# Performance work log

Hardware: AMD Instinct MI355X
Metric: run time of the kernel (lower is better)

## Reference

```python
import jax, jax.numpy as jnp
import numpy as np

B, N, K, C_IN, C_OUT = 8, 24576, 16, 64, 64
BN_EPS = 1e-5


def setup_inputs() -> dict:
    key = jax.random.key(0)
    k1, k2, k3, k4, k5 = jax.random.split(key, 5)
    x = jax.random.normal(k1, (B, N, C_IN), dtype=jnp.float32)
    W = jax.random.normal(k2, (C_OUT, C_IN), dtype=jnp.float32) * 0.05  # Linear weight (no bias)
    # BN affine params; module inits gamma to `init` (0.0) but that zeroes the output,
    # so we use a perturbed gamma for a meaningful correctness baseline.
    gamma = 1.0 + 0.1 * jax.random.normal(k3, (C_OUT,), dtype=jnp.float32)
    beta = 0.1 * jax.random.normal(k4, (C_OUT,), dtype=jnp.float32)
    knn = jax.random.randint(k5, (B, N, K), 0, N, dtype=jnp.int32)
    return {"x": x, "W": W, "gamma": gamma, "beta": beta, "knn": knn}


def _vector_feature(h, knn):
    # h: [B, N, C], knn: [B, N, K] -> max over neighbors of (h_j - h_i): [B, N, C]
    b, n, k = knn.shape
    nbr = jnp.take_along_axis(h, knn.reshape(b, n * k, 1), axis=1).reshape(b, n, k, -1)
    return jnp.max(nbr - h[:, :, None, :], axis=2)


def reference(x, W, gamma, beta, knn):
    h = jnp.einsum('bnc,oc->bno', x, W)            # linear, no bias
    v = _vector_feature(h, knn)                    # knn edge max-pool
    # BatchNorm1d in training mode: batch stats over B*N rows, per channel
    mean = jnp.mean(v, axis=(0, 1))
    var = jnp.mean(jnp.square(v - mean), axis=(0, 1))  # biased variance
    out = (v - mean) * jax.lax.rsqrt(var + BN_EPS) * gamma + beta
    return out
```

## Files before the change

### kernel.cpp

```cpp
#include <hip/hip_runtime.h>
#include <hip/hip_bf16.h>

static constexpr int Bc   = 8;
static constexpr int Nn   = 24576;
static constexpr int Kk   = 16;
static constexpr int Cc   = 64;
static constexpr int Rr   = Bc * Nn;
static constexpr float EPS = 1e-5f;

__global__ __launch_bounds__(256) void linear_kernel(
    const float* __restrict__ x, const float* __restrict__ W,
    __hip_bfloat16* __restrict__ h)
{
    __shared__ float xs[16][64];
    const int tid  = threadIdx.x;
    const int lane = tid & 63;
    const int wave = tid >> 6;

    float w[64];
#pragma unroll
    for (int c4 = 0; c4 < 16; ++c4) {
        float4 t = *reinterpret_cast<const float4*>(&W[lane * 64 + c4 * 4]);
        w[c4 * 4 + 0] = t.x; w[c4 * 4 + 1] = t.y;
        w[c4 * 4 + 2] = t.z; w[c4 * 4 + 3] = t.w;
    }

    const int ntiles = Rr / 16;
    for (int tile = blockIdx.x; tile < ntiles; tile += gridDim.x) {
        const int row0 = tile * 16;
        reinterpret_cast<float4*>(&xs[0][0])[tid] =
            reinterpret_cast<const float4*>(&x[row0 * 64])[tid];
        __syncthreads();
#pragma unroll
        for (int rr = 0; rr < 4; ++rr) {
            const int r = wave * 4 + rr;
            float acc = 0.f;
#pragma unroll
            for (int c4 = 0; c4 < 16; ++c4) {
                float4 t = *reinterpret_cast<const float4*>(&xs[r][c4 * 4]);
                acc = fmaf(t.x, w[c4 * 4 + 0], acc);
                acc = fmaf(t.y, w[c4 * 4 + 1], acc);
                acc = fmaf(t.z, w[c4 * 4 + 2], acc);
                acc = fmaf(t.w, w[c4 * 4 + 3], acc);
            }
            h[(row0 + r) * 64 + lane] = __float2bfloat16(acc);
        }
        __syncthreads();
    }
}

__global__ __launch_bounds__(256) void gather_bn_kernel(
    const __hip_bfloat16* __restrict__ h, const int* __restrict__ knn,
    float* __restrict__ v, float* __restrict__ stats)
{
    const int tid   = threadIdx.x;
    const int lane  = tid & 63;
    const int wave  = tid >> 6;
    const int gwave = blockIdx.x * 4 + wave;
    const int nwav  = gridDim.x * 4;

    float lsum = 0.f, lsq = 0.f;

    for (int row = gwave; row < Rr; row += nwav) {
        const int b     = row / Nn;
        const int bbase = b * Nn;
        const int idx   = knn[row * Kk + (lane & 15)];
        const float hown = __bfloat162float(h[row * 64 + lane]);
        float m = -1e30f;
#pragma unroll
        for (int k = 0; k < Kk; ++k) {
            const int j = __shfl(idx, k);
            m = fmaxf(m, __bfloat162float(h[(bbase + j) * 64 + lane]));
        }
        const float val = m - hown;
        v[row * 64 + lane] = val;
        lsum += val;
        lsq  += val * val;
    }

    __shared__ float s_sum[4][64];
    __shared__ float s_sq[4][64];
    s_sum[wave][lane] = lsum;
    s_sq[wave][lane]  = lsq;
    __syncthreads();
    if (wave == 0) {
        const float a = s_sum[0][lane] + s_sum[1][lane] + s_sum[2][lane] + s_sum[3][lane];
        const float q = s_sq[0][lane]  + s_sq[1][lane]  + s_sq[2][lane]  + s_sq[3][lane];
        atomicAdd(&stats[lane], a);
        atomicAdd(&stats[64 + lane], q);
    }
}

__global__ __launch_bounds__(64) void finalize_stats_kernel(
    const float* __restrict__ stats, const float* __restrict__ gamma,
    const float* __restrict__ beta, float* __restrict__ ss)
{
    const int o = threadIdx.x;
    const float inv_count = 1.0f / (float)Rr;
    const float mean = stats[o] * inv_count;
    const float var  = stats[64 + o] * inv_count - mean * mean;
    const float sc   = gamma[o] * rsqrtf(var + EPS);
    ss[o]      = sc;
    ss[64 + o] = beta[o] - mean * sc;
}

__global__ __launch_bounds__(256) void norm_kernel(
    float* __restrict__ v, const float* __restrict__ ss)
{
    __shared__ float sc[64], sh[64];
    if (threadIdx.x < 64) {
        sc[threadIdx.x] = ss[threadIdx.x];
        sh[threadIdx.x] = ss[64 + threadIdx.x];
    }
    __syncthreads();

    const int total4 = Rr * 64 / 4;
    for (int i = blockIdx.x * blockDim.x + threadIdx.x; i < total4;
         i += gridDim.x * blockDim.x) {
        float4 t = reinterpret_cast<float4*>(v)[i];
        const int c = (i * 4) & 63;
        t.x = t.x * sc[c + 0] + sh[c + 0];
        t.y = t.y * sc[c + 1] + sh[c + 1];
        t.z = t.z * sc[c + 2] + sh[c + 2];
        t.w = t.w * sc[c + 3] + sh[c + 3];
        reinterpret_cast<float4*>(v)[i] = t;
    }
}

extern "C" void kernel_launch(void* const* d_in, const int* in_sizes, int n_in,
                              void* d_out, int out_size, void* d_ws, size_t ws_size,
                              hipStream_t stream)
{
    const float* x     = (const float*)d_in[0];
    const float* W     = (const float*)d_in[1];
    const float* gamma = (const float*)d_in[2];
    const float* beta  = (const float*)d_in[3];
    const int*   knn   = (const int*)d_in[4];
    float*       out   = (float*)d_out;

    __hip_bfloat16* h = (__hip_bfloat16*)d_ws;
    float* stats = (float*)((char*)d_ws + (size_t)Rr * 64 * sizeof(__hip_bfloat16));
    float* ss    = stats + 128;

    hipMemsetAsync(stats, 0, 128 * sizeof(float), stream);

    linear_kernel<<<1024, 256, 0, stream>>>(x, W, h);
    gather_bn_kernel<<<2048, 256, 0, stream>>>(h, knn, out, stats);
    finalize_stats_kernel<<<1, 64, 0, stream>>>(stats, gamma, beta, ss);
    norm_kernel<<<2048, 256, 0, stream>>>(out, ss);
}
```

Before: 237.8 us.

## Use bf16 MFMA for linear, bf16 intermediate v, two-row gather, nontemporal IO

The linear layer is replaced by a per-wave bf16 MFMA 16x16x32 kernel that takes its A fragments straight from global memory, removing the shared-memory staging and scalar FMA loop. The gather kernel now handles two rows per wave iteration to expose more memory-level parallelism and writes v as bf16 into the workspace instead of fp32. The norm kernel reads the bf16 v and writes fp32 output with nontemporal stores. This cuts intermediate traffic, at the cost of extra bf16 rounding on x, W and v, which lowers accuracy.

```diff
diff --git a/kernel.cpp b/kernel.cpp
--- a/kernel.cpp
+++ b/kernel.cpp
@@ -1,5 +1,9 @@
 #include <hip/hip_runtime.h>
 #include <hip/hip_bf16.h>
+
+typedef short s16x8 __attribute__((ext_vector_type(8)));
+typedef float f32x4 __attribute__((ext_vector_type(4)));
+typedef unsigned short u16x8 __attribute__((ext_vector_type(8)));
 
 static constexpr int Bc   = 8;
 static constexpr int Nn   = 24576;
@@ -8,50 +12,83 @@
 static constexpr int Rr   = Bc * Nn;
 static constexpr float EPS = 1e-5f;
 
-__global__ __launch_bounds__(256) void linear_kernel(
+__device__ __forceinline__ unsigned short f2bf(float f) {
+    union { float f; unsigned int u; } c; c.f = f;
+    unsigned int r = c.u + 0x7FFFu + ((c.u >> 16) & 1u);
+    return (unsigned short)(r >> 16);
+}
+__device__ __forceinline__ float bf2f(unsigned short u) {
+    union { unsigned int u; float f; } c; c.u = ((unsigned int)u) << 16; return c.f;
+}
+
+__global__ __launch_bounds__(256) void linear_mfma_kernel(
     const float* __restrict__ x, const float* __restrict__ W,
     __hip_bfloat16* __restrict__ h)
 {
-    __shared__ float xs[16][64];
     const int tid  = threadIdx.x;
-    const int lane = tid & 63;
+    const int l    = tid & 63;
     const int wave = tid >> 6;
-
-    float w[64];
-#pragma unroll
-    for (int c4 = 0; c4 < 16; ++c4) {
-        float4 t = *reinterpret_cast<const float4*>(&W[lane * 64 + c4 * 4]);
-        w[c4 * 4 + 0] = t.x; w[c4 * 4 + 1] = t.y;
-        w[c4 * 4 + 2] = t.z; w[c4 * 4 + 3] = t.w;
-    }
-
+    const int gwave = blockIdx.x * 4 + wave;
+    const int nwav  = gridDim.x * 4;
+
+    const int lr = l & 15;
+    const int kg = (l >> 4) * 8;
+    const int dr = (l >> 4) * 4;
+
+    s16x8 bfrag[4][2];
+#pragma unroll
+    for (int ct = 0; ct < 4; ++ct)
+#pragma unroll
+        for (int kc = 0; kc < 2; ++kc) {
+            const float* bp = W + (ct * 16 + lr) * 64 + kc * 32 + kg;
+            f32x4 b0 = *reinterpret_cast<const f32x4*>(bp);
+            f32x4 b1 = *reinterpret_cast<const f32x4*>(bp + 4);
+            s16x8 f;
+            f[0] = (short)f2bf(b0[0]); f[1] = (short)f2bf(b0[1]);
+            f[2] = (short)f2bf(b0[2]); f[3] = (short)f2bf(b0[3]);
+            f[4] = (short)f2bf(b1[0]); f[5] = (short)f2bf(b1[1]);
+            f[6] = (short)f2bf(b1[2]); f[7] = (short)f2bf(b1[3]);
+            bfrag[ct][kc] = f;
+        }
+
+    unsigned short* hu = (unsigned short*)h;
     const int ntiles = Rr / 16;
-    for (int tile = blockIdx.x; tile < ntiles; tile += gridDim.x) {
-        const int row0 = tile * 16;
-        reinterpret_cast<float4*>(&xs[0][0])[tid] =
-            reinterpret_cast<const float4*>(&x[row0 * 64])[tid];
-        __syncthreads();
-#pragma unroll
-        for (int rr = 0; rr < 4; ++rr) {
-            const int r = wave * 4 + rr;
-            float acc = 0.f;
-#pragma unroll
-            for (int c4 = 0; c4 < 16; ++c4) {
-                float4 t = *reinterpret_cast<const float4*>(&xs[r][c4 * 4]);
-                acc = fmaf(t.x, w[c4 * 4 + 0], acc);
-                acc = fmaf(t.y, w[c4 * 4 + 1], acc);
-                acc = fmaf(t.z, w[c4 * 4 + 2], acc);
-                acc = fmaf(t.w, w[c4 * 4 + 3], acc);
-            }
-            h[(row0 + r) * 64 + lane] = __float2bfloat16(acc);
+    for (int t = gwave; t < ntiles; t += nwav) {
+        const int row0 = t * 16;
+        const float* ap = x + (row0 + lr) * 64 + kg;
+        f32x4 a0 = *reinterpret_cast<const f32x4*>(ap);
+        f32x4 a1 = *reinterpret_cast<const f32x4*>(ap + 4);
+        f32x4 a2 = *reinterpret_cast<const f32x4*>(ap + 32);
+        f32x4 a3 = *reinterpret_cast<const f32x4*>(ap + 36);
+        s16x8 fa0, fa1;
+        fa0[0] = (short)f2bf(a0[0]); fa0[1] = (short)f2bf(a0[1]);
+        fa0[2] = (short)f2bf(a0[2]); fa0[3] = (short)f2bf(a0[3]);
+        fa0[4] = (short)f2bf(a1[0]); fa0[5] = (short)f2bf(a1[1]);
+        fa0[6] = (short)f2bf(a1[2]); fa0[7] = (short)f2bf(a1[3]);
+        fa1[0] = (short)f2bf(a2[0]); fa1[1] = (short)f2bf(a2[1]);
+        fa1[2] = (short)f2bf(a2[2]); fa1[3] = (short)f2bf(a2[3]);
+        fa1[4] = (short)f2bf(a3[0]); fa1[5] = (short)f2bf(a3[1]);
+        fa1[6] = (short)f2bf(a3[2]); fa1[7] = (short)f2bf(a3[3]);
+
+        f32x4 acc[4];
+#pragma unroll
+        for (int ct = 0; ct < 4; ++ct) { acc[ct] = (f32x4){0.f, 0.f, 0.f, 0.f}; }
+#pragma unroll
+        for (int ct = 0; ct < 4; ++ct) {
+            acc[ct] = __builtin_amdgcn_mfma_f32_16x16x32_bf16(fa0, bfrag[ct][0], acc[ct], 0, 0, 0);
+            acc[ct] = __builtin_amdgcn_mfma_f32_16x16x32_bf16(fa1, bfrag[ct][1], acc[ct], 0, 0, 0);
         }
-        __syncthreads();
-    }
-}
-
-__global__ __launch_bounds__(256) void gather_bn_kernel(
+#pragma unroll
+        for (int ct = 0; ct < 4; ++ct)
+#pragma unroll
+            for (int r = 0; r < 4; ++r)
+                hu[(row0 + dr + r) * 64 + ct * 16 + lr] = f2bf(acc[ct][r]);
+    }
+}
+
+__global__ __launch_bounds__(256, 6) void gather_bn_kernel(
     const __hip_bfloat16* __restrict__ h, const int* __restrict__ knn,
-    float* __restrict__ v, float* __restrict__ stats)
+    __hip_bfloat16* __restrict__ v, float* __restrict__ stats)
 {
     const int tid   = threadIdx.x;
     const int lane  = tid & 63;
@@ -59,23 +96,33 @@
     const int gwave = blockIdx.x * 4 + wave;
     const int nwav  = gridDim.x * 4;
 
+    const unsigned short* hu = (const unsigned short*)h;
+    unsigned short* vu = (unsigned short*)v;
+
     float lsum = 0.f, lsq = 0.f;
 
-    for (int row = gwave; row < Rr; row += nwav) {
-        const int b     = row / Nn;
-        const int bbase = b * Nn;
-        const int idx   = knn[row * Kk + (lane & 15)];
-        const float hown = __bfloat162float(h[row * 64 + lane]);
-        float m = -1e30f;
+    for (int r0 = gwave * 2; r0 < Rr; r0 += nwav * 2) {
+        const int row0 = r0, row1 = r0 + 1;
+        const int bbase = (row0 / Nn) * Nn;
+        const int i0 = __builtin_nontemporal_load(&knn[row0 * Kk + (lane & 15)]);
+        const int i1 = __builtin_nontemporal_load(&knn[row1 * Kk + (lane & 15)]);
+        const float o0 = bf2f(hu[row0 * 64 + lane]);
+        const float o1 = bf2f(hu[row1 * 64 + lane]);
+        float m0 = -3e38f, m1 = -3e38f;
 #pragma unroll
         for (int k = 0; k < Kk; ++k) {
-            const int j = __shfl(idx, k);
-            m = fmaxf(m, __bfloat162float(h[(bbase + j) * 64 + lane]));
+            const int j0 = __shfl(i0, k);
+            const int j1 = __shfl(i1, k);
+            const float g0 = bf2f(hu[(bbase + j0) * 64 + lane]);
+            const float g1 = bf2f(hu[(bbase + j1) * 64 + lane]);
+            m0 = fmaxf(m0, g0);
+            m1 = fmaxf(m1, g1);
         }
-        const float val = m - hown;
-        v[row * 64 + lane] = val;
-        lsum += val;
-        lsq  += val * val;
+        const float v0 = m0 - o0, v1 = m1 - o1;
+        __builtin_nontemporal_store(f2bf(v0), &vu[row0 * 64 + lane]);
+        __builtin_nontemporal_store(f2bf(v1), &vu[row1 * 64 + lane]);
+        lsum += v0 + v1;
+        lsq  += v0 * v0 + v1 * v1;
     }
 
     __shared__ float s_sum[4][64];
@@ -105,7 +152,8 @@
 }
 
 __global__ __launch_bounds__(256) void norm_kernel(
-    float* __restrict__ v, const float* __restrict__ ss)
+    const __hip_bfloat16* __restrict__ v, const float* __restrict__ ss,
+    float* __restrict__ out)
 {
     __shared__ float sc[64], sh[64];
     if (threadIdx.x < 64) {
@@ -114,16 +162,24 @@
     }
     __syncthreads();
 
-    const int total4 = Rr * 64 / 4;
-    for (int i = blockIdx.x * blockDim.x + threadIdx.x; i < total4;
+    const u16x8* vu = (const u16x8*)v;
+    const int total8 = Rr * 64 / 8;
+    for (int i = blockIdx.x * blockDim.x + threadIdx.x; i < total8;
          i += gridDim.x * blockDim.x) {
-        float4 t = reinterpret_cast<float4*>(v)[i];
-        const int c = (i * 4) & 63;
-        t.x = t.x * sc[c + 0] + sh[c + 0];
-        t.y = t.y * sc[c + 1] + sh[c + 1];
-        t.z = t.z * sc[c + 2] + sh[c + 2];
-        t.w = t.w * sc[c + 3] + sh[c + 3];
-        reinterpret_cast<float4*>(v)[i] = t;
+        u16x8 t = __builtin_nontemporal_load(&vu[i]);
+        const int c = (i * 8) & 63;
+        f32x4 r0, r1;
+        r0[0] = bf2f(t[0]) * sc[c + 0] + sh[c + 0];
+        r0[1] = bf2f(t[1]) * sc[c + 1] + sh[c + 1];
+        r0[2] = bf2f(t[2]) * sc[c + 2] + sh[c + 2];
+        r0[3] = bf2f(t[3]) * sc[c + 3] + sh[c + 3];
+        r1[0] = bf2f(t[4]) * sc[c + 4] + sh[c + 4];
+        r1[1] = bf2f(t[5]) * sc[c + 5] + sh[c + 5];
+        r1[2] = bf2f(t[6]) * sc[c + 6] + sh[c + 6];
+        r1[3] = bf2f(t[7]) * sc[c + 7] + sh[c + 7];
+        f32x4* op = reinterpret_cast<f32x4*>(out + (size_t)i * 8);
+        __builtin_nontemporal_store(r0, op);
+        __builtin_nontemporal_store(r1, op + 1);
     }
 }
 
@@ -139,13 +195,14 @@
     float*       out   = (float*)d_out;
 
     __hip_bfloat16* h = (__hip_bfloat16*)d_ws;
-    float* stats = (float*)((char*)d_ws + (size_t)Rr * 64 * sizeof(__hip_bfloat16));
+    __hip_bfloat16* v = h + (size_t)Rr * 64;
+    float* stats = (float*)((char*)d_ws + 2 * (size_t)Rr * 64 * sizeof(__hip_bfloat16));
     float* ss    = stats + 128;
 
-    hipMemsetAsync(stats, 0, 128 * sizeof(float), stream);
-
-    linear_kernel<<<1024, 256, 0, stream>>>(x, W, h);
-    gather_bn_kernel<<<2048, 256, 0, stream>>>(h, knn, out, stats);
+    (void)hipMemsetAsync(stats, 0, 128 * sizeof(float), stream);
+
+    linear_mfma_kernel<<<1024, 256, 0, stream>>>(x, W, h);
+    gather_bn_kernel<<<2048, 256, 0, stream>>>(h, knn, v, stats);
     finalize_stats_kernel<<<1, 64, 0, stream>>>(stats, gamma, beta, ss);
-    norm_kernel<<<2048, 256, 0, stream>>>(out, ss);
-}
+    norm_kernel<<<2048, 256, 0, stream>>>(v, ss, out);
+}
```

Result: slower. 288.2 us (+21.2%).
